# Kernel tuning notes

Hardware: AMD Instinct MI355X
Metric: run time of the kernel (lower is better)

## Reference

```python
import jax, jax.numpy as jnp
import numpy as np
import math

NUM_WORDS = 8192
WORD_WIDTH = 512
PROJ_WIDTH = 64
NUM_HEADS = 8
SCALE_FACTOR = 100.0

def setup_inputs() -> dict:
    key = jax.random.key(0)
    kx, kq, kk, kv, ko = jax.random.split(key, 5)
    x = jax.random.normal(kx, (NUM_WORDS, WORD_WIDTH), dtype=jnp.float32)
    w_q = jax.random.normal(kq, (WORD_WIDTH, PROJ_WIDTH), dtype=jnp.float32) / SCALE_FACTOR
    w_k = jax.random.normal(kk, (WORD_WIDTH, PROJ_WIDTH), dtype=jnp.float32) / SCALE_FACTOR
    w_v = jax.random.normal(kv, (WORD_WIDTH, PROJ_WIDTH), dtype=jnp.float32) / SCALE_FACTOR
    w_o = jax.random.normal(ko, (WORD_WIDTH, WORD_WIDTH), dtype=jnp.float32)
    return {"x": x, "w_q": w_q, "w_k": w_k, "w_v": w_v, "w_o": w_o}

def reference(x, w_q, w_k, w_v, w_o):
    # Single self-attention head (all 8 heads in the source share the same weights).
    q = x @ w_q            # [N, P]
    k = x @ w_k            # [N, P]
    v = x @ w_v            # [N, P]
    scores = jax.nn.softmax((q @ k.T) / jnp.sqrt(jnp.float32(q.shape[1])), axis=1)  # [N, N]
    head = scores @ v      # [N, P]
    # concat of NUM_HEADS identical head outputs along dim=1
    concat = jnp.tile(head, (1, NUM_HEADS))  # [N, NUM_HEADS*P]
    return concat @ w_o    # [N, WORD_WIDTH]
```

## Files before the change

kernel.cpp:

```cpp
#include <hip/hip_runtime.h>
#include <stdint.h>

#define N_WORDS 8192
#define LOG2E_8 0.18033688011112043f

typedef __attribute__((ext_vector_type(8))) short short8;
typedef __attribute__((ext_vector_type(4))) float f32x4;
typedef __attribute__((ext_vector_type(4))) _Float16 half4;

__device__ __forceinline__ unsigned short f32_to_bf16(float f) {
    union { float f; unsigned u; } v; v.f = f;
    unsigned u = v.u;
    return (unsigned short)((u + 0x7FFFu + ((u >> 16) & 1u)) >> 16);
}

__device__ __forceinline__ unsigned short f32_to_f16(float f) {
    union { _Float16 h; unsigned short u; } cv;
    cv.h = (_Float16)f;
    return cv.u;
}

__device__ __forceinline__ void async16(const void* g, void* l) {
    __builtin_amdgcn_global_load_lds(
        (const __attribute__((address_space(1))) unsigned int*)g,
        (__attribute__((address_space(3))) unsigned int*)l, 16, 0, 0);
}

__global__ __launch_bounds__(256) void qkv_gemm(
    const float* __restrict__ x,
    const float* __restrict__ wq, const float* __restrict__ wk,
    const float* __restrict__ wv,
    unsigned short* __restrict__ qB, unsigned short* __restrict__ kB,
    unsigned short* __restrict__ vH)
{
    __shared__ __align__(16) unsigned short ldsX[64 * 72];
    __shared__ __align__(16) unsigned short ldsW[64 * 72];

    int t = threadIdx.x;
    int mt = blockIdx.x;
    int mat = blockIdx.y;
    const float* w = (mat == 0) ? wq : (mat == 1) ? wk : wv;

    int wvid = t >> 6, lane = t & 63;
    int lq = lane & 15, quad = lane >> 4;

    f32x4 acc[4];
#pragma unroll
    for (int nt = 0; nt < 4; ++nt) acc[nt] = (f32x4){0.f, 0.f, 0.f, 0.f};

    for (int kb = 0; kb < 8; ++kb) {
        int k0 = kb * 64;
        __syncthreads();
#pragma unroll
        for (int j = 0; j < 4; ++j) {
            int i = t + j * 256;
            int row = i >> 4, c4 = (i & 15) * 4;
            float4 xv = *(const float4*)(x + (size_t)(mt * 64 + row) * 512 + k0 + c4);
            unsigned p0 = f32_to_bf16(xv.x) | ((unsigned)f32_to_bf16(xv.y) << 16);
            unsigned p1 = f32_to_bf16(xv.z) | ((unsigned)f32_to_bf16(xv.w) << 16);
            *(uint2*)(&ldsX[row * 72 + c4]) = make_uint2(p0, p1);
        }
        {
            int n = t & 63, kbs = (t >> 6) * 16;
#pragma unroll
            for (int kk = 0; kk < 16; kk += 2) {
                float a = w[(size_t)(k0 + kbs + kk) * 64 + n];
                float b = w[(size_t)(k0 + kbs + kk + 1) * 64 + n];
                unsigned p = f32_to_bf16(a) | ((unsigned)f32_to_bf16(b) << 16);
                *(unsigned*)(&ldsW[n * 72 + kbs + kk]) = p;
            }
        }
        __syncthreads();

        int m = wvid * 16 + lq;
        short8 a0 = *(const short8*)(&ldsX[m * 72 + quad * 8]);
        short8 a1 = *(const short8*)(&ldsX[m * 72 + 32 + quad * 8]);
#pragma unroll
        for (int nt = 0; nt < 4; ++nt) {
            short8 b0 = *(const short8*)(&ldsW[(nt * 16 + lq) * 72 + quad * 8]);
            short8 b1 = *(const short8*)(&ldsW[(nt * 16 + lq) * 72 + 32 + quad * 8]);
            acc[nt] = __builtin_amdgcn_mfma_f32_16x16x32_bf16(a0, b0, acc[nt], 0, 0, 0);
            acc[nt] = __builtin_amdgcn_mfma_f32_16x16x32_bf16(a1, b1, acc[nt], 0, 0, 0);
        }
    }

    int mrow_base = mt * 64 + wvid * 16;
#pragma unroll
    for (int nt = 0; nt < 4; ++nt) {
#pragma unroll
        for (int r = 0; r < 4; ++r) {
            int row = mrow_base + quad * 4 + r;
            int n = nt * 16 + lq;
            float v = acc[nt][r];
            if (mat == 0) {
                v *= LOG2E_8;
                int col = ((((n >> 3) ^ (row & 7)) << 3)) | (n & 7);
                qB[(size_t)row * 64 + col] = f32_to_bf16(v);
            } else if (mat == 1) {
                int col = ((((n >> 3) ^ (row & 7)) << 3)) | (n & 7);
                kB[(size_t)row * 64 + col] = f32_to_bf16(v);
            } else {
                int rs = (row & ~63) | (((((row >> 3) & 7) ^ (n & 7)) << 3)) | (row & 7);
                vH[(size_t)n * N_WORDS + rs] = f32_to_f16(v);
            }
        }
    }
}

__global__ __launch_bounds__(256) void woeff_kernel(
    const float* __restrict__ wo, float* __restrict__ we)
{
    int i = blockIdx.x * 256 + threadIdx.x;
    int p = i >> 9;
    int j = i & 511;
    float s = 0.0f;
#pragma unroll
    for (int h = 0; h < 8; ++h) s += wo[(size_t)(h * 64 + p) * 512 + j];
    we[i] = s;
}

__global__ __launch_bounds__(256) void attn_kernel(
    const unsigned short* __restrict__ qB,
    const unsigned short* __restrict__ kB,
    const unsigned short* __restrict__ vH,
    float* __restrict__ pO, float* __restrict__ pl, int nk)
{
    __shared__ __align__(16) unsigned short ldsK[128 * 64];
    __shared__ __align__(16) unsigned short ldsV[64 * 128];

    int t = threadIdx.x;
    int wvid = t >> 6, lane = t & 63;
    int lq = lane & 15, quad = lane >> 4;
    int mbase = blockIdx.x * 128 + wvid * 32;
    int n0 = blockIdx.y * nk;

    short8 qf[2][2];
#pragma unroll
    for (int qs = 0; qs < 2; ++qs) {
        int row = mbase + qs * 16 + lq;
        const unsigned short* qr = qB + (size_t)row * 64;
        int s7 = row & 7;
        qf[qs][0] = *(const short8*)(qr + ((quad ^ s7) << 3));
        qf[qs][1] = *(const short8*)(qr + (((4 + quad) ^ s7) << 3));
    }

    f32x4 oacc[2][4];
#pragma unroll
    for (int qs = 0; qs < 2; ++qs)
#pragma unroll
        for (int vt = 0; vt < 4; ++vt) oacc[qs][vt] = (f32x4){0.f, 0.f, 0.f, 0.f};
    float lsum0 = 0.f, lsum1 = 0.f;

    int tiles = nk >> 7;
    for (int tt = 0; tt < tiles; ++tt) {
        int nb = n0 + tt * 128;
        __syncthreads();
        {
            const char* gK = (const char*)kB + (size_t)nb * 128;
#pragma unroll
            for (int i = 0; i < 4; ++i) {
                int L0 = (wvid * 4 + i) * 64;
                async16(gK + (size_t)(L0 + lane) * 16, (char*)ldsK + (size_t)L0 * 16);
            }
#pragma unroll
            for (int i = 0; i < 4; ++i) {
                int L0 = (wvid * 4 + i) * 64;
                int L = L0 + lane;
                int vcol = L >> 4, ct = L & 15;
                const char* src = (const char*)vH + (size_t)vcol * 16384 +
                                  (size_t)nb * 2 + ((ct >> 3) << 7) + ((ct & 7) << 4);
                async16(src, (char*)ldsV + (size_t)L0 * 16);
            }
        }
        __syncthreads();

#pragma unroll 2
        for (int nt = 0; nt < 8; ++nt) {
            int s7 = lq & 7;
            const unsigned short* kr = ldsK + (nt * 16 + lq) * 64;
            short8 a0 = *(const short8*)(kr + ((quad ^ s7) << 3));
            short8 a1 = *(const short8*)(kr + (((4 + quad) ^ s7) << 3));
            f32x4 st0 = (f32x4){0.f, 0.f, 0.f, 0.f};
            f32x4 st1 = (f32x4){0.f, 0.f, 0.f, 0.f};
            st0 = __builtin_amdgcn_mfma_f32_16x16x32_bf16(a0, qf[0][0], st0, 0, 0, 0);
            st0 = __builtin_amdgcn_mfma_f32_16x16x32_bf16(a1, qf[0][1], st0, 0, 0, 0);
            st1 = __builtin_amdgcn_mfma_f32_16x16x32_bf16(a0, qf[1][0], st1, 0, 0, 0);
            st1 = __builtin_amdgcn_mfma_f32_16x16x32_bf16(a1, qf[1][1], st1, 0, 0, 0);

            half4 p0, p1;
#pragma unroll
            for (int r = 0; r < 4; ++r) {
                float e = exp2f(st0[r]);
                lsum0 += e;
                p0[r] = (_Float16)e;
            }
#pragma unroll
            for (int r = 0; r < 4; ++r) {
                float e = exp2f(st1[r]);
                lsum1 += e;
                p1[r] = (_Float16)e;
            }

            int ct = nt * 2 + (quad >> 1);
            int off = (quad & 1) * 4;
#pragma unroll
            for (int vt = 0; vt < 4; ++vt) {
                int vcol = vt * 16 + lq;
                int cs = (ct & 8) | ((ct & 7) ^ (vcol & 7));
                half4 vb = *(const half4*)(ldsV + vcol * 128 + (cs << 3) + off);
                oacc[0][vt] = __builtin_amdgcn_mfma_f32_16x16x16f16(p0, vb, oacc[0][vt], 0, 0, 0);
                oacc[1][vt] = __builtin_amdgcn_mfma_f32_16x16x16f16(p1, vb, oacc[1][vt], 0, 0, 0);
            }
        }
    }

    lsum0 += __shfl_xor(lsum0, 16); lsum0 += __shfl_xor(lsum0, 32);
    lsum1 += __shfl_xor(lsum1, 16); lsum1 += __shfl_xor(lsum1, 32);

    size_t obase = (size_t)blockIdx.y * N_WORDS;
    if (quad == 0) {
        pl[obase + mbase + lq] = lsum0;
        pl[obase + mbase + 16 + lq] = lsum1;
    }
#pragma unroll
    for (int qs = 0; qs < 2; ++qs)
#pragma unroll
        for (int vt = 0; vt < 4; ++vt)
#pragma unroll
            for (int r = 0; r < 4; ++r) {
                int row = mbase + qs * 16 + quad * 4 + r;
                pO[(obase + row) * 64 + vt * 16 + lq] = oacc[qs][vt][r];
            }
}

__global__ __launch_bounds__(256) void combine_kernel(
    const float* __restrict__ pO, const float* __restrict__ pl,
    float* __restrict__ head, int S)
{
    int i = blockIdx.x * 256 + threadIdx.x;
    int row = i >> 6, d = i & 63;
    float so = 0.f, sl = 0.f;
    for (int s = 0; s < S; ++s) {
        so += pO[((size_t)s * N_WORDS + row) * 64 + d];
        sl += pl[(size_t)s * N_WORDS + row];
    }
    head[i] = so / sl;
}

__global__ __launch_bounds__(256) void out_kernel(
    const float* __restrict__ head, const float* __restrict__ we,
    float* __restrict__ out)
{
    __shared__ __align__(16) float ldsHT[64 * 16];
    int t = threadIdx.x;
    int r0 = blockIdx.x * 16;
    {
        int r = t >> 4, c4 = (t & 15) * 4;
        float4 hv = *(const float4*)(head + (size_t)(r0 + r) * 64 + c4);
        ldsHT[(c4 + 0) * 16 + r] = hv.x;
        ldsHT[(c4 + 1) * 16 + r] = hv.y;
        ldsHT[(c4 + 2) * 16 + r] = hv.z;
        ldsHT[(c4 + 3) * 16 + r] = hv.w;
    }
    __syncthreads();

    int w = t >> 6, l = t & 63;
    int cg = w & 1, rg = w >> 1;
    int j0 = cg * 256 + l * 4;

    float4 acc[8];
#pragma unroll
    for (int rr = 0; rr < 8; ++rr) acc[rr] = (float4){0.f, 0.f, 0.f, 0.f};

    for (int k = 0; k < 64; ++k) {
        float4 wv = *(const float4*)(we + (size_t)k * 512 + j0);
        float4 h0 = *(const float4*)(ldsHT + k * 16 + rg * 8);
        float4 h1 = *(const float4*)(ldsHT + k * 16 + rg * 8 + 4);
        float hr[8] = {h0.x, h0.y, h0.z, h0.w, h1.x, h1.y, h1.z, h1.w};
#pragma unroll
        for (int rr = 0; rr < 8; ++rr) {
            acc[rr].x = fmaf(hr[rr], wv.x, acc[rr].x);
            acc[rr].y = fmaf(hr[rr], wv.y, acc[rr].y);
            acc[rr].z = fmaf(hr[rr], wv.z, acc[rr].z);
            acc[rr].w = fmaf(hr[rr], wv.w, acc[rr].w);
        }
    }

#pragma unroll
    for (int rr = 0; rr < 8; ++rr) {
        int row = r0 + rg * 8 + rr;
        *(float4*)(out + (size_t)row * 512 + j0) = acc[rr];
    }
}

extern "C" void kernel_launch(void* const* d_in, const int* in_sizes, int n_in,
                              void* d_out, int out_size, void* d_ws, size_t ws_size,
                              hipStream_t stream)
{
    const float* x  = (const float*)d_in[0];
    const float* wq = (const float*)d_in[1];
    const float* wk = (const float*)d_in[2];
    const float* wv = (const float*)d_in[3];
    const float* wo = (const float*)d_in[4];
    float* out = (float*)d_out;

    char* ws = (char*)d_ws;
    unsigned short* qB = (unsigned short*)(ws);
    unsigned short* kB = (unsigned short*)(ws + 1048576);
    unsigned short* vH = (unsigned short*)(ws + 2097152);
    float* we   = (float*)(ws + 3145728);
    float* head = (float*)(ws + 3276800);
    float* pl   = (float*)(ws + 5373952);
    float* pO   = (float*)(ws + 5636096);

    int S = (ws_size >= (size_t)(5636096) + 8u * 2097152u) ? 8 : 4;
    int nk = N_WORDS / S;

    hipLaunchKernelGGL(qkv_gemm, dim3(128, 3), dim3(256), 0, stream,
                       x, wq, wk, wv, qB, kB, vH);
    hipLaunchKernelGGL(woeff_kernel, dim3(128), dim3(256), 0, stream, wo, we);
    hipLaunchKernelGGL(attn_kernel, dim3(64, S), dim3(256), 0, stream,
                       qB, kB, vH, pO, pl, nk);
    hipLaunchKernelGGL(combine_kernel, dim3(2048), dim3(256), 0, stream,
                       pO, pl, head, S);
    hipLaunchKernelGGL(out_kernel, dim3(512), dim3(256), 0, stream,
                       head, we, out);
}
```

Measured before the change: 137.1 us.

## Double-buffer attention tiles, fuse kernels, and use wider MFMA for PV

```diff
diff --git a/kernel.cpp b/kernel.cpp
--- a/kernel.cpp
+++ b/kernel.cpp
@@ -6,7 +6,9 @@
 
 typedef __attribute__((ext_vector_type(8))) short short8;
 typedef __attribute__((ext_vector_type(4))) float f32x4;
+typedef __attribute__((ext_vector_type(2))) __fp16 pkhalf2;
 typedef __attribute__((ext_vector_type(4))) _Float16 half4;
+typedef __attribute__((ext_vector_type(8))) _Float16 half8;
 
 __device__ __forceinline__ unsigned short f32_to_bf16(float f) {
     union { float f; unsigned u; } v; v.f = f;
@@ -29,16 +31,28 @@
 __global__ __launch_bounds__(256) void qkv_gemm(
     const float* __restrict__ x,
     const float* __restrict__ wq, const float* __restrict__ wk,
-    const float* __restrict__ wv,
+    const float* __restrict__ wv, const float* __restrict__ wo,
     unsigned short* __restrict__ qB, unsigned short* __restrict__ kB,
-    unsigned short* __restrict__ vH)
+    unsigned short* __restrict__ vH, float* __restrict__ we)
 {
+    int t = threadIdx.x;
+    int mat = blockIdx.y;
+
+    if (mat == 3) {
+        int i = blockIdx.x * 256 + t;
+        int p = i >> 9;
+        int j = i & 511;
+        float s = 0.0f;
+#pragma unroll
+        for (int h = 0; h < 8; ++h) s += wo[(size_t)(h * 64 + p) * 512 + j];
+        we[i] = s;
+        return;
+    }
+
     __shared__ __align__(16) unsigned short ldsX[64 * 72];
     __shared__ __align__(16) unsigned short ldsW[64 * 72];
 
-    int t = threadIdx.x;
     int mt = blockIdx.x;
-    int mat = blockIdx.y;
     const float* w = (mat == 0) ? wq : (mat == 1) ? wk : wv;
 
     int wvid = t >> 6, lane = t & 63;
@@ -48,29 +62,52 @@
 #pragma unroll
     for (int nt = 0; nt < 4; ++nt) acc[nt] = (f32x4){0.f, 0.f, 0.f, 0.f};
 
+    float4 xr[4];
+    float wr[16];
+    int wn = t & 63, wkbs = (t >> 6) * 16;
+
+    {
+        int k0 = 0;
+#pragma unroll
+        for (int j2 = 0; j2 < 4; ++j2) {
+            int i = t + j2 * 256;
+            int row = i >> 4, c4 = (i & 15) * 4;
+            xr[j2] = *(const float4*)(x + (size_t)(mt * 64 + row) * 512 + k0 + c4);
+        }
+#pragma unroll
+        for (int kk = 0; kk < 16; ++kk)
+            wr[kk] = w[(size_t)(k0 + wkbs + kk) * 64 + wn];
+    }
+
     for (int kb = 0; kb < 8; ++kb) {
-        int k0 = kb * 64;
         __syncthreads();
 #pragma unroll
-        for (int j = 0; j < 4; ++j) {
-            int i = t + j * 256;
+        for (int j2 = 0; j2 < 4; ++j2) {
+            int i = t + j2 * 256;
             int row = i >> 4, c4 = (i & 15) * 4;
-            float4 xv = *(const float4*)(x + (size_t)(mt * 64 + row) * 512 + k0 + c4);
-            unsigned p0 = f32_to_bf16(xv.x) | ((unsigned)f32_to_bf16(xv.y) << 16);
-            unsigned p1 = f32_to_bf16(xv.z) | ((unsigned)f32_to_bf16(xv.w) << 16);
+            unsigned p0 = f32_to_bf16(xr[j2].x) | ((unsigned)f32_to_bf16(xr[j2].y) << 16);
+            unsigned p1 = f32_to_bf16(xr[j2].z) | ((unsigned)f32_to_bf16(xr[j2].w) << 16);
             *(uint2*)(&ldsX[row * 72 + c4]) = make_uint2(p0, p1);
         }
-        {
-            int n = t & 63, kbs = (t >> 6) * 16;
-#pragma unroll
-            for (int kk = 0; kk < 16; kk += 2) {
-                float a = w[(size_t)(k0 + kbs + kk) * 64 + n];
-                float b = w[(size_t)(k0 + kbs + kk + 1) * 64 + n];
-                unsigned p = f32_to_bf16(a) | ((unsigned)f32_to_bf16(b) << 16);
-                *(unsigned*)(&ldsW[n * 72 + kbs + kk]) = p;
-            }
+#pragma unroll
+        for (int kk = 0; kk < 16; kk += 2) {
+            unsigned p = f32_to_bf16(wr[kk]) | ((unsigned)f32_to_bf16(wr[kk + 1]) << 16);
+            *(unsigned*)(&ldsW[wn * 72 + wkbs + kk]) = p;
         }
         __syncthreads();
+
+        if (kb < 7) {
+            int k0 = (kb + 1) * 64;
+#pragma unroll
+            for (int j2 = 0; j2 < 4; ++j2) {
+                int i = t + j2 * 256;
+                int row = i >> 4, c4 = (i & 15) * 4;
+                xr[j2] = *(const float4*)(x + (size_t)(mt * 64 + row) * 512 + k0 + c4);
+            }
+#pragma unroll
+            for (int kk = 0; kk < 16; ++kk)
+                wr[kk] = w[(size_t)(k0 + wkbs + kk) * 64 + wn];
+        }
 
         int m = wvid * 16 + lq;
         short8 a0 = *(const short8*)(&ldsX[m * 72 + quad * 8]);
@@ -107,26 +144,14 @@
     }
 }
 
-__global__ __launch_bounds__(256) void woeff_kernel(
-    const float* __restrict__ wo, float* __restrict__ we)
-{
-    int i = blockIdx.x * 256 + threadIdx.x;
-    int p = i >> 9;
-    int j = i & 511;
-    float s = 0.0f;
-#pragma unroll
-    for (int h = 0; h < 8; ++h) s += wo[(size_t)(h * 64 + p) * 512 + j];
-    we[i] = s;
-}
-
 __global__ __launch_bounds__(256) void attn_kernel(
     const unsigned short* __restrict__ qB,
     const unsigned short* __restrict__ kB,
     const unsigned short* __restrict__ vH,
     float* __restrict__ pO, float* __restrict__ pl, int nk)
 {
-    __shared__ __align__(16) unsigned short ldsK[128 * 64];
-    __shared__ __align__(16) unsigned short ldsV[64 * 128];
+    __shared__ __align__(16) unsigned short ldsK[2][128 * 64];
+    __shared__ __align__(16) unsigned short ldsV[2][64 * 128];
 
     int t = threadIdx.x;
     int wvid = t >> 6, lane = t & 63;
@@ -149,78 +174,107 @@
     for (int qs = 0; qs < 2; ++qs)
 #pragma unroll
         for (int vt = 0; vt < 4; ++vt) oacc[qs][vt] = (f32x4){0.f, 0.f, 0.f, 0.f};
-    float lsum0 = 0.f, lsum1 = 0.f;
+    f32x4 lacc[2];
+    lacc[0] = (f32x4){0.f, 0.f, 0.f, 0.f};
+    lacc[1] = (f32x4){0.f, 0.f, 0.f, 0.f};
+
+    const half8 ones = {(_Float16)1.f, (_Float16)1.f, (_Float16)1.f, (_Float16)1.f,
+                        (_Float16)1.f, (_Float16)1.f, (_Float16)1.f, (_Float16)1.f};
+
+    auto stage = [&](int buf, int nb) {
+        const char* gK = (const char*)kB + (size_t)nb * 128;
+#pragma unroll
+        for (int i = 0; i < 4; ++i) {
+            int L0 = (wvid * 4 + i) * 64;
+            async16(gK + (size_t)(L0 + lane) * 16, (char*)ldsK[buf] + (size_t)L0 * 16);
+        }
+#pragma unroll
+        for (int i = 0; i < 4; ++i) {
+            int L0 = (wvid * 4 + i) * 64;
+            int L = L0 + lane;
+            int vcol = L >> 4, ct = L & 15;
+            const char* src = (const char*)vH + (size_t)vcol * 16384 +
+                              (size_t)nb * 2 + ((ct >> 3) << 7) + ((ct & 7) << 4);
+            async16(src, (char*)ldsV[buf] + (size_t)L0 * 16);
+        }
+    };
 
     int tiles = nk >> 7;
+    stage(0, n0);
+    int cur = 0;
+
     for (int tt = 0; tt < tiles; ++tt) {
-        int nb = n0 + tt * 128;
         __syncthreads();
-        {
-            const char* gK = (const char*)kB + (size_t)nb * 128;
-#pragma unroll
-            for (int i = 0; i < 4; ++i) {
-                int L0 = (wvid * 4 + i) * 64;
-                async16(gK + (size_t)(L0 + lane) * 16, (char*)ldsK + (size_t)L0 * 16);
-            }
-#pragma unroll
-            for (int i = 0; i < 4; ++i) {
-                int L0 = (wvid * 4 + i) * 64;
-                int L = L0 + lane;
-                int vcol = L >> 4, ct = L & 15;
-                const char* src = (const char*)vH + (size_t)vcol * 16384 +
-                                  (size_t)nb * 2 + ((ct >> 3) << 7) + ((ct & 7) << 4);
-                async16(src, (char*)ldsV + (size_t)L0 * 16);
-            }
-        }
-        __syncthreads();
-
-#pragma unroll 2
-        for (int nt = 0; nt < 8; ++nt) {
-            int s7 = lq & 7;
-            const unsigned short* kr = ldsK + (nt * 16 + lq) * 64;
-            short8 a0 = *(const short8*)(kr + ((quad ^ s7) << 3));
-            short8 a1 = *(const short8*)(kr + (((4 + quad) ^ s7) << 3));
-            f32x4 st0 = (f32x4){0.f, 0.f, 0.f, 0.f};
-            f32x4 st1 = (f32x4){0.f, 0.f, 0.f, 0.f};
-            st0 = __builtin_amdgcn_mfma_f32_16x16x32_bf16(a0, qf[0][0], st0, 0, 0, 0);
-            st0 = __builtin_amdgcn_mfma_f32_16x16x32_bf16(a1, qf[0][1], st0, 0, 0, 0);
-            st1 = __builtin_amdgcn_mfma_f32_16x16x32_bf16(a0, qf[1][0], st1, 0, 0, 0);
-            st1 = __builtin_amdgcn_mfma_f32_16x16x32_bf16(a1, qf[1][1], st1, 0, 0, 0);
-
-            half4 p0, p1;
-#pragma unroll
-            for (int r = 0; r < 4; ++r) {
-                float e = exp2f(st0[r]);
-                lsum0 += e;
-                p0[r] = (_Float16)e;
-            }
-#pragma unroll
-            for (int r = 0; r < 4; ++r) {
-                float e = exp2f(st1[r]);
-                lsum1 += e;
-                p1[r] = (_Float16)e;
-            }
-
-            int ct = nt * 2 + (quad >> 1);
+        if (tt + 1 < tiles) stage(cur ^ 1, n0 + (tt + 1) * 128);
+
+        __builtin_amdgcn_s_setprio(1);
+        const unsigned short* K = ldsK[cur];
+        const unsigned short* V = ldsV[cur];
+
+#pragma unroll
+        for (int u = 0; u < 4; ++u) {
+            f32x4 st[2][2];
+#pragma unroll
+            for (int h = 0; h < 2; ++h) {
+                int nt = 2 * u + h;
+                int s7 = lq & 7;
+                const unsigned short* kr = K + (nt * 16 + lq) * 64;
+                short8 a0 = *(const short8*)(kr + ((quad ^ s7) << 3));
+                short8 a1 = *(const short8*)(kr + (((4 + quad) ^ s7) << 3));
+                f32x4 s0 = (f32x4){0.f, 0.f, 0.f, 0.f};
+                f32x4 s1 = (f32x4){0.f, 0.f, 0.f, 0.f};
+                s0 = __builtin_amdgcn_mfma_f32_16x16x32_bf16(a0, qf[0][0], s0, 0, 0, 0);
+                s0 = __builtin_amdgcn_mfma_f32_16x16x32_bf16(a1, qf[0][1], s0, 0, 0, 0);
+                s1 = __builtin_amdgcn_mfma_f32_16x16x32_bf16(a0, qf[1][0], s1, 0, 0, 0);
+                s1 = __builtin_amdgcn_mfma_f32_16x16x32_bf16(a1, qf[1][1], s1, 0, 0, 0);
+                st[h][0] = s0;
+                st[h][1] = s1;
+            }
+
+            union { half8 v8; pkhalf2 v2[4]; } pa[2];
+#pragma unroll
+            for (int qs = 0; qs < 2; ++qs) {
+#pragma unroll
+                for (int h = 0; h < 2; ++h) {
+                    float e0 = exp2f(st[h][qs][0]);
+                    float e1 = exp2f(st[h][qs][1]);
+                    float e2 = exp2f(st[h][qs][2]);
+                    float e3 = exp2f(st[h][qs][3]);
+                    pa[qs].v2[h * 2 + 0] = __builtin_amdgcn_cvt_pkrtz(e0, e1);
+                    pa[qs].v2[h * 2 + 1] = __builtin_amdgcn_cvt_pkrtz(e2, e3);
+                }
+                lacc[qs] = __builtin_amdgcn_mfma_f32_16x16x32_f16(
+                    pa[qs].v8, ones, lacc[qs], 0, 0, 0);
+            }
+
+            int ct0 = 4 * u + (quad >> 1);
             int off = (quad & 1) * 4;
 #pragma unroll
             for (int vt = 0; vt < 4; ++vt) {
                 int vcol = vt * 16 + lq;
-                int cs = (ct & 8) | ((ct & 7) ^ (vcol & 7));
-                half4 vb = *(const half4*)(ldsV + vcol * 128 + (cs << 3) + off);
-                oacc[0][vt] = __builtin_amdgcn_mfma_f32_16x16x16f16(p0, vb, oacc[0][vt], 0, 0, 0);
-                oacc[1][vt] = __builtin_amdgcn_mfma_f32_16x16x16f16(p1, vb, oacc[1][vt], 0, 0, 0);
-            }
-        }
-    }
-
-    lsum0 += __shfl_xor(lsum0, 16); lsum0 += __shfl_xor(lsum0, 32);
-    lsum1 += __shfl_xor(lsum1, 16); lsum1 += __shfl_xor(lsum1, 32);
+                int cs0 = (ct0 & 8) | ((ct0 & 7) ^ (vcol & 7));
+                int ct1 = ct0 + 2;
+                int cs1 = (ct1 & 8) | ((ct1 & 7) ^ (vcol & 7));
+                union { half8 v8; half4 v4[2]; } vb;
+                vb.v4[0] = *(const half4*)(V + vcol * 128 + (cs0 << 3) + off);
+                vb.v4[1] = *(const half4*)(V + vcol * 128 + (cs1 << 3) + off);
+                oacc[0][vt] = __builtin_amdgcn_mfma_f32_16x16x32_f16(
+                    pa[0].v8, vb.v8, oacc[0][vt], 0, 0, 0);
+                oacc[1][vt] = __builtin_amdgcn_mfma_f32_16x16x32_f16(
+                    pa[1].v8, vb.v8, oacc[1][vt], 0, 0, 0);
+            }
+        }
+        __builtin_amdgcn_s_setprio(0);
+        cur ^= 1;
+    }
 
     size_t obase = (size_t)blockIdx.y * N_WORDS;
-    if (quad == 0) {
-        pl[obase + mbase + lq] = lsum0;
-        pl[obase + mbase + 16 + lq] = lsum1;
+    if (lq == 0) {
+#pragma unroll
+        for (int qs = 0; qs < 2; ++qs)
+#pragma unroll
+            for (int r = 0; r < 4; ++r)
+                pl[obase + mbase + qs * 16 + quad * 4 + r] = lacc[qs][r];
     }
 #pragma unroll
     for (int qs = 0; qs < 2; ++qs)
@@ -233,34 +287,24 @@
             }
 }
 
-__global__ __launch_bounds__(256) void combine_kernel(
+__global__ __launch_bounds__(256) void out_kernel(
     const float* __restrict__ pO, const float* __restrict__ pl,
-    float* __restrict__ head, int S)
-{
-    int i = blockIdx.x * 256 + threadIdx.x;
-    int row = i >> 6, d = i & 63;
-    float so = 0.f, sl = 0.f;
-    for (int s = 0; s < S; ++s) {
-        so += pO[((size_t)s * N_WORDS + row) * 64 + d];
-        sl += pl[(size_t)s * N_WORDS + row];
-    }
-    head[i] = so / sl;
-}
-
-__global__ __launch_bounds__(256) void out_kernel(
-    const float* __restrict__ head, const float* __restrict__ we,
-    float* __restrict__ out)
+    const float* __restrict__ we, float* __restrict__ out, int S)
 {
     __shared__ __align__(16) float ldsHT[64 * 16];
     int t = threadIdx.x;
     int r0 = blockIdx.x * 16;
-    {
-        int r = t >> 4, c4 = (t & 15) * 4;
-        float4 hv = *(const float4*)(head + (size_t)(r0 + r) * 64 + c4);
-        ldsHT[(c4 + 0) * 16 + r] = hv.x;
-        ldsHT[(c4 + 1) * 16 + r] = hv.y;
-        ldsHT[(c4 + 2) * 16 + r] = hv.z;
-        ldsHT[(c4 + 3) * 16 + r] = hv.w;
+
+#pragma unroll
+    for (int j = 0; j < 4; ++j) {
+        int i = t + j * 256;
+        int row = i >> 6, d = i & 63;
+        float so = 0.f, sl = 0.f;
+        for (int s = 0; s < S; ++s) {
+            so += pO[((size_t)s * N_WORDS + r0 + row) * 64 + d];
+            sl += pl[(size_t)s * N_WORDS + r0 + row];
+        }
+        ldsHT[d * 16 + row] = so / sl;
     }
     __syncthreads();
 
@@ -309,20 +353,16 @@
     unsigned short* kB = (unsigned short*)(ws + 1048576);
     unsigned short* vH = (unsigned short*)(ws + 2097152);
     float* we   = (float*)(ws + 3145728);
-    float* head = (float*)(ws + 3276800);
     float* pl   = (float*)(ws + 5373952);
     float* pO   = (float*)(ws + 5636096);
 
     int S = (ws_size >= (size_t)(5636096) + 8u * 2097152u) ? 8 : 4;
     int nk = N_WORDS / S;
 
-    hipLaunchKernelGGL(qkv_gemm, dim3(128, 3), dim3(256), 0, stream,
-                       x, wq, wk, wv, qB, kB, vH);
-    hipLaunchKernelGGL(woeff_kernel, dim3(128), dim3(256), 0, stream, wo, we);
+    hipLaunchKernelGGL(qkv_gemm, dim3(128, 4), dim3(256), 0, stream,
+                       x, wq, wk, wv, wo, qB, kB, vH, we);
     hipLaunchKernelGGL(attn_kernel, dim3(64, S), dim3(256), 0, stream,
                        qB, kB, vH, pO, pl, nk);
-    hipLaunchKernelGGL(combine_kernel, dim3(2048), dim3(256), 0, stream,
-                       pO, pl, head, S);
     hipLaunchKernelGGL(out_kernel, dim3(512), dim3(256), 0, stream,
-                       head, we, out);
-}
+                       pO, pl, we, out, S);
+}
```

After: 131.8 us. -3.9%, faster.
